# Performance work log

Measured on AMD Instinct MI355X. Metric: run time of the kernel, lower is better.

Reference implementation:

```python
import jax, jax.numpy as jnp
import numpy as np

BLOCK = 128          # fp8 quantization block size (from linear_deepseek_v3)
FP8_MAX = 448.0      # max representable value of float8_e4m3fn
F8 = jnp.float8_e4m3fn
G, T, K, N = 8, 1024, 7168, 2048


def setup_inputs() -> dict:
    key = jax.random.key(0)
    kx, kw, kb = jax.random.split(key, 3)
    xs = jax.random.normal(kx, (G, T, K), jnp.float32)
    # Build an fp8 block-quantized weight + per-(128x128)-block fp32 scale,
    # matching the stored self.weight (fp8) and self.scale parameters.
    w_raw = jax.random.normal(kw, (G, N, K), jnp.float32)
    wb = w_raw.reshape(G, N // BLOCK, BLOCK, K // BLOCK, BLOCK)
    amax = jnp.max(jnp.abs(wb), axis=(2, 4))            # [G, NB, KB]
    scale = amax / FP8_MAX
    w_q = (wb / scale[:, :, None, :, None]).astype(F8).astype(jnp.float32)
    weight = w_q.reshape(G, N, K)                        # fp8 code values held in fp32
    bias = jax.random.normal(kb, (G, N), jnp.float32) * 0.02
    return {"xs": xs, "weight": weight, "scale": scale, "bias": bias}


def reference(xs, weight, scale, bias):
    """Grouped fp8 block-quantized GEMM with inline dequant.
    xs:     [G, T, K] fp32 activations (one slab per group)
    weight: [G, N, K] fp8-quantized weights (stored as fp32 code values)
    scale:  [G, N/128, K/128] fp32 per-block weight scales
    bias:   [G, N] fp32
    """
    g, t, k = xs.shape
    n = weight.shape[1]
    kb, nb = k // BLOCK, n // BLOCK
    # --- act_quant_deepseek_v3: per (token, 128-col block) absmax/448 scale ---
    xb = xs.reshape(g, t, kb, BLOCK)
    a_scale = jnp.max(jnp.abs(xb), axis=-1) / FP8_MAX        # [G, T, KB]
    x_q = (xb / a_scale[..., None]).astype(F8).astype(jnp.float32)
    x_deq = (x_q * a_scale[..., None]).reshape(g, t, k)      # fused dequant
    # --- weight dequant: broadcast per-(128x128)-block scale ---
    w_deq = (weight.reshape(g, nb, BLOCK, kb, BLOCK)
             * scale[:, :, None, :, None]).reshape(g, n, k)
    # --- grouped GEMM (y = x A^T) + bias, fp32 accumulation ---
    y = jnp.einsum('gtk,gnk->gtn', x_deq, w_deq) + bias[:, None, :]
    return y
```

## Files before the change

### kernel.cpp

```cpp
#include <hip/hip_runtime.h>
#include <hip/hip_bf16.h>
#include <stdint.h>

#define G_ 8
#define T_ 1024
#define K_ 7168
#define N_ 2048
#define KB_ (K_/128)
#define NB_ (N_/128)
#define NT8_ 56

#define ACT_WGS  57344
#define WREC_WGS 28672

typedef __attribute__((ext_vector_type(4))) float f32x4;
typedef __attribute__((ext_vector_type(8))) int   i32x8;

typedef __attribute__((address_space(3))) uint32_t lds_u32_t;
typedef const __attribute__((address_space(1))) uint32_t gbl_u32_t;

__device__ __forceinline__ void gload_lds16(const void* gsrc, const void* ldst)
{
    __builtin_amdgcn_global_load_lds(
        (gbl_u32_t*)(uintptr_t)gsrc,
        (lds_u32_t*)(uint32_t)(uintptr_t)ldst, 16, 0, 0);
}

__device__ __forceinline__ void blockbar()
{
    asm volatile("" ::: "memory");
    __builtin_amdgcn_s_barrier();
    asm volatile("" ::: "memory");
}

__global__ __launch_bounds__(256) void prep_kernel(
    const float* __restrict__ xs, uint8_t* __restrict__ xq8,
    float* __restrict__ ascale,
    const float* __restrict__ w, uint8_t* __restrict__ wq8)
{
    const int bid = blockIdx.x;
    if (bid < ACT_WGS) {
        const int grp = (bid * 256 + threadIdx.x) >> 5;
        const int l   = threadIdx.x & 31;
        const size_t base = (size_t)grp * 128 + (size_t)l * 4;

        const float4 v = *(const float4*)(xs + base);
        float am = fmaxf(fmaxf(fabsf(v.x), fabsf(v.y)),
                         fmaxf(fabsf(v.z), fabsf(v.w)));
#pragma unroll
        for (int off = 1; off <= 16; off <<= 1)
            am = fmaxf(am, __shfl_xor(am, off, 64));

        const float rs = 448.0f / am;
        const float s  = am * (1.0f / 448.0f);

        int pk = __builtin_amdgcn_cvt_pk_fp8_f32(v.x * rs, v.y * rs, 0, false);
        pk     = __builtin_amdgcn_cvt_pk_fp8_f32(v.z * rs, v.w * rs, pk, true);
        *(uint32_t*)(xq8 + base) = (uint32_t)pk;

        if (l == 0) {
            const int kb = grp % KB_;
            const int t  = (grp / KB_) & (T_ - 1);
            const int g  = grp / (KB_ * T_);
            ascale[(((size_t)(g * 4 + (t >> 8))) * KB_ + kb) * 256 + (t & 255)] = s;
        }
    } else {
        const size_t i = ((size_t)(bid - ACT_WGS) * 256 + threadIdx.x) * 16;
        uint32_t o[4];
#pragma unroll
        for (int q = 0; q < 4; ++q) {
            const float4 a = *(const float4*)(w + i + q * 4);
            int pk = __builtin_amdgcn_cvt_pk_fp8_f32(a.x, a.y, 0, false);
            pk     = __builtin_amdgcn_cvt_pk_fp8_f32(a.z, a.w, pk, true);
            o[q] = (uint32_t)pk;
        }
        *(uint4*)(wq8 + i) = make_uint4(o[0], o[1], o[2], o[3]);
    }
}

union Frag { i32x8 v; struct { int4 lo, hi; } p; };

#define RD_A(mh)                                                              \
  { _Pragma("unroll") for (int m = 0; m < 4; ++m) {                           \
      const int r  = wrow + ((mh)*4 + m)*16 + l15;                            \
      const int rx = (r & 7) << 4;                                            \
      const char* bp = smem + cb*32768 + r*128;                               \
      aF[m].p.lo = *(const int4*)(bp + ((lhi*32) ^ rx));                      \
      aF[m].p.hi = *(const int4*)(bp + ((lhi*32 + 16) ^ rx));                 \
      const float4 sv = *(const float4*)(smem + 131072 + ((u>>3)&1)*8192 +    \
          (u & 7)*1024 + (wrow + ((mh)*4 + m)*16 + lhi*4)*4);                 \
      asw[m][0] = sv.x*wsc; asw[m][1] = sv.y*wsc;                             \
      asw[m][2] = sv.z*wsc; asw[m][3] = sv.w*wsc;                             \
  } }

#define RD_B(nh)                                                              \
  { _Pragma("unroll") for (int n = 0; n < 2; ++n) {                           \
      const int r  = wcol + ((nh)*2 + n)*16 + l15;                            \
      const int rx = (r & 7) << 4;                                            \
      const char* bp = smem + 65536 + cb*32768 + r*128;                       \
      bF[(nh)*2+n].p.lo = *(const int4*)(bp + ((lhi*32) ^ rx));               \
      bF[(nh)*2+n].p.hi = *(const int4*)(bp + ((lhi*32 + 16) ^ rx));          \
  } }

#define MM(mh, nh)                                                            \
  { _Pragma("unroll") for (int m = 0; m < 4; ++m) {                           \
      _Pragma("unroll") for (int n = 0; n < 2; ++n) {                         \
        f32x4 blk = __builtin_amdgcn_mfma_scale_f32_16x16x128_f8f6f4(         \
            aF[m].v, bF[(nh)*2+n].v, z4, 0, 0,                                \
            0, 0x7F7F7F7F, 0, 0x7F7F7F7F);                                    \
        _Pragma("unroll") for (int j = 0; j < 4; ++j)                         \
          acc[(mh)*4+m][(nh)*2+n][j] += blk[j] * asw[m][j];                   \
  } } }

#define STG_A8(c, t, b) gload_lds16(pA8[c] + (size_t)(t)*128,                 \
      smem + (b)*32768 + (c)*8192 + tid*16)
#define STG_B8(c, t, b) gload_lds16(pB8[c] + (size_t)(t)*128,                 \
      smem + 65536 + (b)*32768 + (c)*8192 + tid*16)
#define STG_S(c) gload_lds16(pS + (size_t)(c)*2048,                           \
      smem + 131072 + ((c)&1)*8192 + tid*16)

__global__ __launch_bounds__(512) void gemm_fp8_kernel(
    const uint8_t* __restrict__ xq8, const uint8_t* __restrict__ wq8,
    const float* __restrict__ ascale, const float* __restrict__ wscale,
    const float* __restrict__ bias, float* __restrict__ y)
{
    __shared__ char smem[147968];

    const int bx0 = blockIdx.x;
    const int bx  = (bx0 & 7) * 32 + (bx0 >> 3);
    const int g   = bx >> 5;
    const int tm  = (bx >> 3) & 3;
    const int tn  = bx & 7;
    const int t0  = tm * 256, n0 = tn * 256;

    const int tid = threadIdx.x, lane = tid & 63, wid = tid >> 6;
    const int l15 = lane & 15, lhi = lane >> 4;
    const int wrow = (wid >> 2) * 128;
    const int wcol = (wid & 3) * 64;

    const uint8_t* Ag = xq8 + (size_t)g * T_ * K_;
    const uint8_t* Bg = wq8 + (size_t)g * N_ * K_;

    const int srow = tid >> 3;
    const int xoff = ((tid & 7) ^ (srow & 7)) * 16;
    const uint8_t* pA8[4];
    const uint8_t* pB8[4];
#pragma unroll
    for (int c = 0; c < 4; ++c) {
        pA8[c] = Ag + (size_t)(t0 + c * 64 + srow) * K_ + xoff;
        pB8[c] = Bg + (size_t)(n0 + c * 64 + srow) * K_ + xoff;
    }
    const float* pS = ascale + ((size_t)(g * 4 + tm) * KB_) * 256 + tid * 4;

    const f32x4 z4 = {0.f, 0.f, 0.f, 0.f};
    f32x4 acc[8][4] = {};
    Frag aF[4], bF[4];
    float asw[4][4];

    if (tid < 2 * KB_) {
        const float v = wscale[((size_t)(g * NB_ + tn * 2)) * KB_ + tid];
        *(float*)(smem + 147456 + tid * 4) = v;
    }
    STG_S(0);
#pragma unroll
    for (int c = 0; c < 4; ++c) { STG_A8(c, 0, 0); STG_B8(c, 0, 0); }
#pragma unroll
    for (int c = 0; c < 4; ++c) { STG_A8(c, 1, 1); STG_B8(c, 1, 1); }
    asm volatile("s_waitcnt vmcnt(8)" ::: "memory");
    asm volatile("s_waitcnt lgkmcnt(0)" ::: "memory");
    blockbar();

    const int wsoff = 147456 + ((wcol >> 7) * KB_) * 4;

    for (int u = 0; u < NT8_; ++u) {
        const int cb = u & 1;
        const bool pf = (u + 2 < NT8_);
        const float wsc = *(const float*)(smem + wsoff + u * 4);

        if ((u & 7) == 0 && u + 8 < NT8_) STG_S((u >> 3) + 1);
        RD_A(0); RD_B(0);
        blockbar();
        asm volatile("s_waitcnt lgkmcnt(0)" ::: "memory");
        __builtin_amdgcn_s_setprio(1);
        MM(0, 0);
        __builtin_amdgcn_s_setprio(0);
        blockbar();

        RD_B(1);
        if (pf) { STG_A8(0, u + 2, cb); STG_A8(2, u + 2, cb); }
        blockbar();
        asm volatile("s_waitcnt lgkmcnt(0)" ::: "memory");
        __builtin_amdgcn_s_setprio(1);
        MM(0, 1);
        __builtin_amdgcn_s_setprio(0);
        blockbar();

        RD_A(1);
        if (pf) { STG_B8(0, u + 2, cb); STG_B8(1, u + 2, cb); }
        blockbar();
        asm volatile("s_waitcnt lgkmcnt(0)" ::: "memory");
        __builtin_amdgcn_s_setprio(1);
        MM(1, 0);
        __builtin_amdgcn_s_setprio(0);
        blockbar();

        if (pf) { STG_A8(1, u + 2, cb); STG_A8(3, u + 2, cb);
                  STG_B8(2, u + 2, cb); STG_B8(3, u + 2, cb); }
        __builtin_amdgcn_s_setprio(1);
        MM(1, 1);
        __builtin_amdgcn_s_setprio(0);
        if (pf)                  asm volatile("s_waitcnt vmcnt(8)" ::: "memory");
        else if (u + 1 < NT8_)   asm volatile("s_waitcnt vmcnt(0)" ::: "memory");
        blockbar();
    }

    float* Yg = y + (size_t)g * T_ * N_;
#pragma unroll
    for (int n = 0; n < 4; ++n) {
        const int col = n0 + wcol + n * 16 + l15;
        const float bv = bias[g * N_ + col];
#pragma unroll
        for (int m = 0; m < 8; ++m) {
            const int r0 = t0 + wrow + m * 16 + lhi * 4;
#pragma unroll
            for (int j = 0; j < 4; ++j)
                Yg[(size_t)(r0 + j) * N_ + col] = acc[m][n][j] + bv;
        }
    }
}

extern "C" void kernel_launch(void* const* d_in, const int* in_sizes, int n_in,
                              void* d_out, int out_size, void* d_ws, size_t ws_size,
                              hipStream_t stream)
{
    const float* xs     = (const float*)d_in[0];
    const float* weight = (const float*)d_in[1];
    const float* scale  = (const float*)d_in[2];
    const float* bias   = (const float*)d_in[3];
    float* y = (float*)d_out;

    uint8_t* xq8  = (uint8_t*)d_ws;
    float*   ascl = (float*)((char*)d_ws + 58720256);
    uint8_t* wq8  = (uint8_t*)((char*)d_ws + 60555264);

    prep_kernel<<<ACT_WGS + WREC_WGS, 256, 0, stream>>>(
        xs, xq8, ascl, weight, wq8);

    gemm_fp8_kernel<<<256, 512, 0, stream>>>(xq8, wq8, ascl, scale, bias, y);
}
```

Before: 360.7 us.

## Fuse weight fp8 conversion into GEMM and shrink tiles to 128x128

Removes the separate weight-requantization pass: the GEMM now loads the fp32 weights directly, converts them to fp8 in registers and writes them to LDS, so the fp8 weight copy is never written to or read back from global memory. Tiles shrink from 256x256 with 512 threads to 128x128 with 256 threads and two blocks per CU, giving 1024 workgroups. The main loop becomes double-buffered with one barrier per K-step instead of several. In exchange, the fp32 weight reads are four times larger per byte of fp8 used and are re-read by each of the 8 row tiles rather than 4. The smaller tiles also lower arithmetic intensity.

```diff
diff --git a/kernel.cpp b/kernel.cpp
--- a/kernel.cpp
+++ b/kernel.cpp
@@ -6,12 +6,9 @@
 #define T_ 1024
 #define K_ 7168
 #define N_ 2048
-#define KB_ (K_/128)
-#define NB_ (N_/128)
+#define KB_ 56
+#define NB_ 16
 #define NT8_ 56
-
-#define ACT_WGS  57344
-#define WREC_WGS 28672
 
 typedef __attribute__((ext_vector_type(4))) float f32x4;
 typedef __attribute__((ext_vector_type(8))) int   i32x8;
@@ -33,185 +30,163 @@
     asm volatile("" ::: "memory");
 }
 
-__global__ __launch_bounds__(256) void prep_kernel(
+__global__ __launch_bounds__(256) void act_quant_kernel(
     const float* __restrict__ xs, uint8_t* __restrict__ xq8,
-    float* __restrict__ ascale,
-    const float* __restrict__ w, uint8_t* __restrict__ wq8)
-{
-    const int bid = blockIdx.x;
-    if (bid < ACT_WGS) {
-        const int grp = (bid * 256 + threadIdx.x) >> 5;
-        const int l   = threadIdx.x & 31;
-        const size_t base = (size_t)grp * 128 + (size_t)l * 4;
-
-        const float4 v = *(const float4*)(xs + base);
-        float am = fmaxf(fmaxf(fabsf(v.x), fabsf(v.y)),
-                         fmaxf(fabsf(v.z), fabsf(v.w)));
-#pragma unroll
-        for (int off = 1; off <= 16; off <<= 1)
-            am = fmaxf(am, __shfl_xor(am, off, 64));
-
-        const float rs = 448.0f / am;
-        const float s  = am * (1.0f / 448.0f);
-
-        int pk = __builtin_amdgcn_cvt_pk_fp8_f32(v.x * rs, v.y * rs, 0, false);
-        pk     = __builtin_amdgcn_cvt_pk_fp8_f32(v.z * rs, v.w * rs, pk, true);
-        *(uint32_t*)(xq8 + base) = (uint32_t)pk;
-
-        if (l == 0) {
-            const int kb = grp % KB_;
-            const int t  = (grp / KB_) & (T_ - 1);
-            const int g  = grp / (KB_ * T_);
-            ascale[(((size_t)(g * 4 + (t >> 8))) * KB_ + kb) * 256 + (t & 255)] = s;
-        }
-    } else {
-        const size_t i = ((size_t)(bid - ACT_WGS) * 256 + threadIdx.x) * 16;
-        uint32_t o[4];
-#pragma unroll
-        for (int q = 0; q < 4; ++q) {
-            const float4 a = *(const float4*)(w + i + q * 4);
-            int pk = __builtin_amdgcn_cvt_pk_fp8_f32(a.x, a.y, 0, false);
-            pk     = __builtin_amdgcn_cvt_pk_fp8_f32(a.z, a.w, pk, true);
-            o[q] = (uint32_t)pk;
-        }
-        *(uint4*)(wq8 + i) = make_uint4(o[0], o[1], o[2], o[3]);
+    float* __restrict__ ascale)
+{
+    const int grp = (blockIdx.x * 256 + threadIdx.x) >> 5;
+    const int l   = threadIdx.x & 31;
+    const size_t base = (size_t)grp * 128 + (size_t)l * 4;
+
+    const float4 v = *(const float4*)(xs + base);
+    float am = fmaxf(fmaxf(fabsf(v.x), fabsf(v.y)),
+                     fmaxf(fabsf(v.z), fabsf(v.w)));
+#pragma unroll
+    for (int off = 1; off <= 16; off <<= 1)
+        am = fmaxf(am, __shfl_xor(am, off, 64));
+
+    const float rs = 448.0f / am;
+    const float s  = am * (1.0f / 448.0f);
+
+    int pk = __builtin_amdgcn_cvt_pk_fp8_f32(v.x * rs, v.y * rs, 0, false);
+    pk     = __builtin_amdgcn_cvt_pk_fp8_f32(v.z * rs, v.w * rs, pk, true);
+    *(uint32_t*)(xq8 + base) = (uint32_t)pk;
+
+    if (l == 0) {
+        const int kb = grp % KB_;
+        const int t  = (grp / KB_) & (T_ - 1);
+        const int g  = grp / (KB_ * T_);
+        ascale[(((size_t)(g * 4 + (t >> 8))) * KB_ + kb) * 256 + (t & 255)] = s;
     }
 }
 
 union Frag { i32x8 v; struct { int4 lo, hi; } p; };
 
-#define RD_A(mh)                                                              \
-  { _Pragma("unroll") for (int m = 0; m < 4; ++m) {                           \
-      const int r  = wrow + ((mh)*4 + m)*16 + l15;                            \
-      const int rx = (r & 7) << 4;                                            \
-      const char* bp = smem + cb*32768 + r*128;                               \
-      aF[m].p.lo = *(const int4*)(bp + ((lhi*32) ^ rx));                      \
-      aF[m].p.hi = *(const int4*)(bp + ((lhi*32 + 16) ^ rx));                 \
-      const float4 sv = *(const float4*)(smem + 131072 + ((u>>3)&1)*8192 +    \
-          (u & 7)*1024 + (wrow + ((mh)*4 + m)*16 + lhi*4)*4);                 \
-      asw[m][0] = sv.x*wsc; asw[m][1] = sv.y*wsc;                             \
-      asw[m][2] = sv.z*wsc; asw[m][3] = sv.w*wsc;                             \
+#define RD_FRAG(dst, base, r)                                                 \
+  { const int rx_ = ((r) & 7) << 4;                                           \
+    const char* bp_ = smem + (base) + (r)*128;                                \
+    dst.p.lo = *(const int4*)(bp_ + ((lhi*32) ^ rx_));                        \
+    dst.p.hi = *(const int4*)(bp_ + ((lhi*32 + 16) ^ rx_)); }
+
+#define STG_A(c, t, bb) gload_lds16(pA8[c] + (size_t)(t)*128,                 \
+      smem + (bb)*16384 + (c)*4096 + tid*16)
+#define STG_S(c) gload_lds16(pS + (size_t)(c)*2048,                           \
+      smem + 65536 + ((c)&1)*4096 + tid*16)
+
+#define LOAD_B(t)                                                             \
+  { _Pragma("unroll") for (int i = 0; i < 16; ++i)                            \
+      br[i] = *(const f32x4*)(pWb + (size_t)(t)*128 + (size_t)i*(2*K_)); }
+
+#define CVT_WRITE_B(bb)                                                       \
+  { _Pragma("unroll") for (int i = 0; i < 16; ++i) {                          \
+      int pk_ = __builtin_amdgcn_cvt_pk_fp8_f32(br[i][0], br[i][1], 0, false);\
+      pk_ = __builtin_amdgcn_cvt_pk_fp8_f32(br[i][2], br[i][3], pk_, true);   \
+      const int r_ = wid*32 + i*2 + lp;                                       \
+      *(uint32_t*)(smem + 32768 + (bb)*16384 + r_*128 +                       \
+          (((l31 >> 2) ^ (r_ & 7)) << 4) + (l31 & 3)*4) = (uint32_t)pk_;      \
   } }
 
-#define RD_B(nh)                                                              \
-  { _Pragma("unroll") for (int n = 0; n < 2; ++n) {                           \
-      const int r  = wcol + ((nh)*2 + n)*16 + l15;                            \
-      const int rx = (r & 7) << 4;                                            \
-      const char* bp = smem + 65536 + cb*32768 + r*128;                       \
-      bF[(nh)*2+n].p.lo = *(const int4*)(bp + ((lhi*32) ^ rx));               \
-      bF[(nh)*2+n].p.hi = *(const int4*)(bp + ((lhi*32 + 16) ^ rx));          \
-  } }
-
-#define MM(mh, nh)                                                            \
-  { _Pragma("unroll") for (int m = 0; m < 4; ++m) {                           \
-      _Pragma("unroll") for (int n = 0; n < 2; ++n) {                         \
-        f32x4 blk = __builtin_amdgcn_mfma_scale_f32_16x16x128_f8f6f4(         \
-            aF[m].v, bF[(nh)*2+n].v, z4, 0, 0,                                \
-            0, 0x7F7F7F7F, 0, 0x7F7F7F7F);                                    \
-        _Pragma("unroll") for (int j = 0; j < 4; ++j)                         \
-          acc[(mh)*4+m][(nh)*2+n][j] += blk[j] * asw[m][j];                   \
-  } } }
-
-#define STG_A8(c, t, b) gload_lds16(pA8[c] + (size_t)(t)*128,                 \
-      smem + (b)*32768 + (c)*8192 + tid*16)
-#define STG_B8(c, t, b) gload_lds16(pB8[c] + (size_t)(t)*128,                 \
-      smem + 65536 + (b)*32768 + (c)*8192 + tid*16)
-#define STG_S(c) gload_lds16(pS + (size_t)(c)*2048,                           \
-      smem + 131072 + ((c)&1)*8192 + tid*16)
-
-__global__ __launch_bounds__(512) void gemm_fp8_kernel(
-    const uint8_t* __restrict__ xq8, const uint8_t* __restrict__ wq8,
+__global__ __launch_bounds__(256, 2) void gemm_fp8_kernel(
+    const uint8_t* __restrict__ xq8, const float* __restrict__ w,
     const float* __restrict__ ascale, const float* __restrict__ wscale,
     const float* __restrict__ bias, float* __restrict__ y)
 {
-    __shared__ char smem[147968];
+    __shared__ char smem[73984];
 
     const int bx0 = blockIdx.x;
-    const int bx  = (bx0 & 7) * 32 + (bx0 >> 3);
-    const int g   = bx >> 5;
-    const int tm  = (bx >> 3) & 3;
-    const int tn  = bx & 7;
-    const int t0  = tm * 256, n0 = tn * 256;
+    const int g     = bx0 & 7;
+    const int inner = bx0 >> 3;
+    const int tn    = inner >> 3;
+    const int tm    = inner & 7;
+    const int t0 = tm * 128, n0 = tn * 128;
 
     const int tid = threadIdx.x, lane = tid & 63, wid = tid >> 6;
     const int l15 = lane & 15, lhi = lane >> 4;
-    const int wrow = (wid >> 2) * 128;
-    const int wcol = (wid & 3) * 64;
+    const int l31 = lane & 31, lp = lane >> 5;
+    const int wrow = (wid >> 1) * 64;
+    const int wcol = (wid & 1) * 64;
 
     const uint8_t* Ag = xq8 + (size_t)g * T_ * K_;
-    const uint8_t* Bg = wq8 + (size_t)g * N_ * K_;
-
-    const int srow = tid >> 3;
-    const int xoff = ((tid & 7) ^ (srow & 7)) * 16;
+    const float*   Wg = w   + (size_t)g * N_ * K_;
+
     const uint8_t* pA8[4];
-    const uint8_t* pB8[4];
-#pragma unroll
-    for (int c = 0; c < 4; ++c) {
-        pA8[c] = Ag + (size_t)(t0 + c * 64 + srow) * K_ + xoff;
-        pB8[c] = Bg + (size_t)(n0 + c * 64 + srow) * K_ + xoff;
-    }
-    const float* pS = ascale + ((size_t)(g * 4 + tm) * KB_) * 256 + tid * 4;
+#pragma unroll
+    for (int c = 0; c < 4; ++c)
+        pA8[c] = Ag + (size_t)(t0 + c * 32 + (tid >> 3)) * K_
+                    + ((tid & 7) ^ ((tid >> 3) & 7)) * 16;
+
+    const float* pWb = Wg + (size_t)(n0 + wid * 32 + lp) * K_ + l31 * 4;
+
+    const float* pS = ascale + ((size_t)(g * 4 + (tm >> 1)) * KB_) * 256
+                    + (tid >> 5) * 256 + (tm & 1) * 128 + (tid & 31) * 4;
 
     const f32x4 z4 = {0.f, 0.f, 0.f, 0.f};
-    f32x4 acc[8][4] = {};
-    Frag aF[4], bF[4];
-    float asw[4][4];
-
-    if (tid < 2 * KB_) {
-        const float v = wscale[((size_t)(g * NB_ + tn * 2)) * KB_ + tid];
-        *(float*)(smem + 147456 + tid * 4) = v;
-    }
+    f32x4 acc[4][4] = {};
+    Frag bF[4];
+    f32x4 br[16];
+
+    if (tid < KB_) {
+        const float wv = wscale[((size_t)(g * NB_ + tn)) * KB_ + tid];
+        *(float*)(smem + 73728 + tid * 4) = wv;
+    }
+    LOAD_B(0);
+    asm volatile("s_waitcnt vmcnt(0)" ::: "memory");
+    CVT_WRITE_B(0);
+#pragma unroll
+    for (int c = 0; c < 4; ++c) STG_A(c, 0, 0);
     STG_S(0);
-#pragma unroll
-    for (int c = 0; c < 4; ++c) { STG_A8(c, 0, 0); STG_B8(c, 0, 0); }
-#pragma unroll
-    for (int c = 0; c < 4; ++c) { STG_A8(c, 1, 1); STG_B8(c, 1, 1); }
-    asm volatile("s_waitcnt vmcnt(8)" ::: "memory");
+    asm volatile("s_waitcnt vmcnt(0)" ::: "memory");
     asm volatile("s_waitcnt lgkmcnt(0)" ::: "memory");
     blockbar();
 
-    const int wsoff = 147456 + ((wcol >> 7) * KB_) * 4;
-
     for (int u = 0; u < NT8_; ++u) {
-        const int cb = u & 1;
-        const bool pf = (u + 2 < NT8_);
-        const float wsc = *(const float*)(smem + wsoff + u * 4);
+        const int cur = u & 1, nxt = cur ^ 1;
+        const bool pf = (u + 1 < NT8_);
+        const int abuf = (u >> 3) & 1;
 
         if ((u & 7) == 0 && u + 8 < NT8_) STG_S((u >> 3) + 1);
-        RD_A(0); RD_B(0);
-        blockbar();
+        if (pf) {
+            LOAD_B(u + 1);
+#pragma unroll
+            for (int c = 0; c < 4; ++c) STG_A(c, u + 1, nxt);
+        }
+
+        const float wsc = *(const float*)(smem + 73728 + u * 4);
+
+#pragma unroll
+        for (int n = 0; n < 4; ++n)
+            RD_FRAG(bF[n], 32768 + cur * 16384, wcol + n * 16 + l15);
+
         asm volatile("s_waitcnt lgkmcnt(0)" ::: "memory");
         __builtin_amdgcn_s_setprio(1);
-        MM(0, 0);
+#pragma unroll
+        for (int m = 0; m < 4; ++m) {
+            Frag aF;
+            const int r = wrow + m * 16 + l15;
+            RD_FRAG(aF, cur * 16384, r);
+            const float4 sv = *(const float4*)(smem + 65536 + abuf * 4096 +
+                (u & 7) * 512 + (wrow + m * 16 + lhi * 4) * 4);
+            const float a0 = sv.x * wsc, a1 = sv.y * wsc,
+                        a2 = sv.z * wsc, a3 = sv.w * wsc;
+#pragma unroll
+            for (int n = 0; n < 4; ++n) {
+                f32x4 blk = __builtin_amdgcn_mfma_scale_f32_16x16x128_f8f6f4(
+                    aF.v, bF[n].v, z4, 0, 0, 0, 0x7F7F7F7F, 0, 0x7F7F7F7F);
+                acc[m][n][0] += blk[0] * a0;
+                acc[m][n][1] += blk[1] * a1;
+                acc[m][n][2] += blk[2] * a2;
+                acc[m][n][3] += blk[3] * a3;
+            }
+        }
         __builtin_amdgcn_s_setprio(0);
-        blockbar();
-
-        RD_B(1);
-        if (pf) { STG_A8(0, u + 2, cb); STG_A8(2, u + 2, cb); }
-        blockbar();
-        asm volatile("s_waitcnt lgkmcnt(0)" ::: "memory");
-        __builtin_amdgcn_s_setprio(1);
-        MM(0, 1);
-        __builtin_amdgcn_s_setprio(0);
-        blockbar();
-
-        RD_A(1);
-        if (pf) { STG_B8(0, u + 2, cb); STG_B8(1, u + 2, cb); }
-        blockbar();
-        asm volatile("s_waitcnt lgkmcnt(0)" ::: "memory");
-        __builtin_amdgcn_s_setprio(1);
-        MM(1, 0);
-        __builtin_amdgcn_s_setprio(0);
-        blockbar();
-
-        if (pf) { STG_A8(1, u + 2, cb); STG_A8(3, u + 2, cb);
-                  STG_B8(2, u + 2, cb); STG_B8(3, u + 2, cb); }
-        __builtin_amdgcn_s_setprio(1);
-        MM(1, 1);
-        __builtin_amdgcn_s_setprio(0);
-        if (pf)                  asm volatile("s_waitcnt vmcnt(8)" ::: "memory");
-        else if (u + 1 < NT8_)   asm volatile("s_waitcnt vmcnt(0)" ::: "memory");
-        blockbar();
+
+        if (pf) {
+            asm volatile("s_waitcnt vmcnt(4)" ::: "memory");
+            CVT_WRITE_B(nxt);
+            asm volatile("s_waitcnt vmcnt(0)" ::: "memory");
+            asm volatile("s_waitcnt lgkmcnt(0)" ::: "memory");
+            blockbar();
+        }
     }
 
     float* Yg = y + (size_t)g * T_ * N_;
@@ -220,7 +195,7 @@
         const int col = n0 + wcol + n * 16 + l15;
         const float bv = bias[g * N_ + col];
 #pragma unroll
-        for (int m = 0; m < 8; ++m) {
+        for (int m = 0; m < 4; ++m) {
             const int r0 = t0 + wrow + m * 16 + lhi * 4;
 #pragma unroll
             for (int j = 0; j < 4; ++j)
@@ -241,10 +216,8 @@
 
     uint8_t* xq8  = (uint8_t*)d_ws;
     float*   ascl = (float*)((char*)d_ws + 58720256);
-    uint8_t* wq8  = (uint8_t*)((char*)d_ws + 60555264);
-
-    prep_kernel<<<ACT_WGS + WREC_WGS, 256, 0, stream>>>(
-        xs, xq8, ascl, weight, wq8);
-
-    gemm_fp8_kernel<<<256, 512, 0, stream>>>(xq8, wq8, ascl, scale, bias, y);
-}
+
+    act_quant_kernel<<<(G_ * T_ * KB_) / 8, 256, 0, stream>>>(xs, xq8, ascl);
+    gemm_fp8_kernel<<<G_ * (T_ / 128) * (N_ / 128), 256, 0, stream>>>(
+        xq8, weight, ascl, scale, bias, y);
+}
```

New measurement: 394.4 us. 9.3% more time.
